# Optimization experiments

Hardware: AMD Instinct MI355X
Metric: run time of the kernel (lower is better)

The kernel has to match this reference:

```python
import jax, jax.numpy as jnp
import numpy as np
import math

EPS = 1e-5
BN_SCALE = 1.0 / math.sqrt(1.0 + EPS)  # eval BatchNorm with running mean 0, var 1


def _ln(x, g, b):
    m = jnp.mean(x, axis=-1, keepdims=True)
    v = jnp.mean((x - m) ** 2, axis=-1, keepdims=True)
    return (x - m) * jax.lax.rsqrt(v + EPS) * g + b


def _swish(x):
    return x * jax.nn.sigmoid(x)


def _ffn(x, ng, nb, w1, b1, w2, b2):
    h = _ln(x, ng, nb)
    h = _swish(h @ w1.T + b1)
    return h @ w2.T + b2


def _mhsa(x, a_ng, a_nb, qkv_w, qkv_b, rel_w, out_w, out_b):
    B, T, D = x.shape
    H, hd = rel_w.shape  # rel_pos_proj: Linear(head_dim, num_heads), weight [H, hd]
    h = _ln(x, a_ng, a_nb)
    qkv = (h @ qkv_w.T + qkv_b).reshape(B, T, 3, H, hd)
    q = qkv[:, :, 0].transpose(0, 2, 1, 3)  # [B,H,T,hd]
    k = qkv[:, :, 1].transpose(0, 2, 1, 3)
    v = qkv[:, :, 2].transpose(0, 2, 1, 3)
    scores = jnp.einsum('bhqd,bhkd->bhqk', q, k) * (hd ** -0.5)
    # relative sinusoidal PE over 2T-1 offsets
    pos = jnp.arange(-(T - 1), T, dtype=x.dtype)[:, None]
    div = jnp.exp(jnp.arange(0, hd, 2, dtype=x.dtype) * (-math.log(10000.0) / hd))
    ang = pos * div  # [2T-1, hd/2]
    pe = jnp.zeros((2 * T - 1, hd), dtype=x.dtype)
    pe = pe.at[:, 0::2].set(jnp.sin(ang)).at[:, 1::2].set(jnp.cos(ang))
    rel_bias = pe @ rel_w.T  # [2T-1, H]
    idx = jnp.arange(T)[:, None] - jnp.arange(T)[None, :] + (T - 1)  # [T,T]
    bias = rel_bias[idx].transpose(2, 0, 1)  # [H,T,T]
    attn = jax.nn.softmax(scores + bias[None], axis=-1)
    o = jnp.einsum('bhqk,bhkd->bhqd', attn, v).transpose(0, 2, 1, 3).reshape(B, T, D)
    return o @ out_w.T + out_b


def _conv(x, c_ng, c_nb, pw1_w, pw1_b, dw_w, dw_b, bn_g, bn_b, pw2_w, pw2_b):
    B, T, D = x.shape
    K = dw_w.shape[1]
    h = _ln(x, c_ng, c_nb)
    h = h @ pw1_w.T + pw1_b  # pointwise conv == linear, [B,T,2D]
    a, g = jnp.split(h, 2, axis=-1)
    h = a * jax.nn.sigmoid(g)  # GLU, [B,T,D]
    h = h.transpose(0, 2, 1)  # [B,D,T]
    h = jax.lax.conv_general_dilated(
        h, dw_w[:, None, :], window_strides=(1,), padding=[(K // 2, K // 2)],
        dimension_numbers=('NCH', 'OIH', 'NCH'), feature_group_count=D) + dw_b[:, None]
    h = h * (BN_SCALE * bn_g)[:, None] + bn_b[:, None]  # eval-mode BatchNorm1d
    h = _swish(h)
    h = h.transpose(0, 2, 1)  # [B,T,D]
    return h @ pw2_w.T + pw2_b


def _forward(x, g_ffn1, b_ffn1, g_mhsa, b_mhsa, g_conv, b_conv, g_ffn2, b_ffn2, g_out, b_out,
             f1_ng, f1_nb, f1_w1, f1_b1, f1_w2, f1_b2,
             f2_ng, f2_nb, f2_w1, f2_b1, f2_w2, f2_b2,
             a_ng, a_nb, qkv_w, qkv_b, rel_w, out_w, out_b,
             c_ng, c_nb, pw1_w, pw1_b, dw_w, dw_b, bn_g, bn_b, pw2_w, pw2_b):
    x = x + 0.5 * _ffn(_ln(x, g_ffn1, b_ffn1), f1_ng, f1_nb, f1_w1, f1_b1, f1_w2, f1_b2)
    x = x + _mhsa(_ln(x, g_mhsa, b_mhsa), a_ng, a_nb, qkv_w, qkv_b, rel_w, out_w, out_b)
    x = x + _conv(_ln(x, g_conv, b_conv), c_ng, c_nb, pw1_w, pw1_b, dw_w, dw_b, bn_g, bn_b, pw2_w, pw2_b)
    x = _ln(x + 0.5 * _ffn(_ln(x, g_ffn2, b_ffn2), f2_ng, f2_nb, f2_w1, f2_b1, f2_w2, f2_b2), g_out, b_out)
    return x


def setup_inputs() -> dict:
    key = jax.random.key(0)
    B, T, D, H, F, K = 8, 2048, 256, 4, 1024, 31
    ks = iter(jax.random.split(key, 16))
    w = lambda shape, s: jax.random.normal(next(ks), shape, jnp.float32) * s
    d = {}
    d['x'] = w((B, T, D), 1.0)
    for n in ['g_ffn1', 'g_mhsa', 'g_conv', 'g_ffn2', 'g_out', 'f1_ng', 'f2_ng', 'a_ng', 'c_ng', 'bn_g']:
        d[n] = jnp.ones((D,), jnp.float32)
    for n in ['b_ffn1', 'b_mhsa', 'b_conv', 'b_ffn2', 'b_out', 'f1_nb', 'f2_nb', 'a_nb', 'c_nb', 'bn_b']:
        d[n] = jnp.zeros((D,), jnp.float32)
    d['f1_w1'] = w((F, D), 0.05); d['f1_b1'] = jnp.zeros((F,), jnp.float32)
    d['f1_w2'] = w((D, F), 0.03); d['f1_b2'] = jnp.zeros((D,), jnp.float32)
    d['f2_w1'] = w((F, D), 0.05); d['f2_b1'] = jnp.zeros((F,), jnp.float32)
    d['f2_w2'] = w((D, F), 0.03); d['f2_b2'] = jnp.zeros((D,), jnp.float32)
    d['qkv_w'] = w((3 * D, D), 0.05); d['qkv_b'] = jnp.zeros((3 * D,), jnp.float32)
    d['rel_w'] = w((H, D // H), 0.05)
    d['out_w'] = w((D, D), 0.05); d['out_b'] = jnp.zeros((D,), jnp.float32)
    d['pw1_w'] = w((2 * D, D), 0.05); d['pw1_b'] = jnp.zeros((2 * D,), jnp.float32)
    d['dw_w'] = w((D, K), 0.1); d['dw_b'] = jnp.zeros((D,), jnp.float32)
    d['pw2_w'] = w((D, D), 0.05); d['pw2_b'] = jnp.zeros((D,), jnp.float32)
    return d


def reference(x, g_ffn1, b_ffn1, g_mhsa, b_mhsa, g_conv, b_conv, g_ffn2, b_ffn2, g_out, b_out,
              f1_ng, f1_nb, f1_w1, f1_b1, f1_w2, f1_b2,
              f2_ng, f2_nb, f2_w1, f2_b1, f2_w2, f2_b2,
              a_ng, a_nb, qkv_w, qkv_b, rel_w, out_w, out_b,
              c_ng, c_nb, pw1_w, pw1_b, dw_w, dw_b, bn_g, bn_b, pw2_w, pw2_b):
    return _forward(x, g_ffn1, b_ffn1, g_mhsa, b_mhsa, g_conv, b_conv, g_ffn2, b_ffn2, g_out, b_out,
                    f1_ng, f1_nb, f1_w1, f1_b1, f1_w2, f1_b2,
                    f2_ng, f2_nb, f2_w1, f2_b1, f2_w2, f2_b2,
                    a_ng, a_nb, qkv_w, qkv_b, rel_w, out_w, out_b,
                    c_ng, c_nb, pw1_w, pw1_b, dw_w, dw_b, bn_g, bn_b, pw2_w, pw2_b)
```

## Files before the change

kernel.cpp:

```cpp
#include <hip/hip_runtime.h>
#include <math.h>


typedef _Float16 half8 __attribute__((ext_vector_type(8)));
typedef _Float16 half4v __attribute__((ext_vector_type(4)));
typedef float floatx4 __attribute__((ext_vector_type(4)));

#define LN_EPS 1e-5f
#define BN_SCALE 0.9999950000374996f

__device__ __forceinline__ void async_copy16(const _Float16* g, _Float16* l) {
    __builtin_amdgcn_global_load_lds(
        (const __attribute__((address_space(1))) void*)g,
        (__attribute__((address_space(3))) void*)l, 16, 0, 0);
}

__global__ __launch_bounds__(256) void cast_kernel(const float* __restrict__ s,
                                                   _Float16* __restrict__ d, int n) {
    int i = blockIdx.x * 256 + threadIdx.x;
    if (i < n) d[i] = (_Float16)s[i];
}

__global__ __launch_bounds__(256) void cast_pw1_kernel(const float* __restrict__ w,
        const float* __restrict__ b, _Float16* __restrict__ wp, float* __restrict__ bp) {
    int i = blockIdx.x * 256 + threadIdx.x;
    int p = i >> 8, c = i & 255;
    int chunk = p >> 4, within = p & 15;
    int orig = ((chunk & 1) ? 256 : 0) + (chunk >> 1) * 16 + within;
    wp[i] = (_Float16)w[orig * 256 + c];
    if (c == 0) bp[p] = b[orig];
}

__global__ __launch_bounds__(256) void ln2_kernel(const float* __restrict__ x,
        const float* __restrict__ g1, const float* __restrict__ b1,
        const float* __restrict__ g2, const float* __restrict__ b2,
        _Float16* __restrict__ y) {
    int wave = threadIdx.x >> 6, lane = threadIdx.x & 63;
    size_t row = (size_t)blockIdx.x * 4 + wave;
    float4 v = ((const float4*)(x + row * 256))[lane];
    float s = v.x + v.y + v.z + v.w;
    float s2 = v.x * v.x + v.y * v.y + v.z * v.z + v.w * v.w;
    #pragma unroll
    for (int m = 1; m < 64; m <<= 1) { s += __shfl_xor(s, m, 64); s2 += __shfl_xor(s2, m, 64); }
    float mean = s * (1.f / 256.f);
    float var = s2 * (1.f / 256.f) - mean * mean;
    float rs = rsqrtf(var + LN_EPS);
    int c0 = lane * 4;
    float y0 = (v.x - mean) * rs * g1[c0 + 0] + b1[c0 + 0];
    float y1 = (v.y - mean) * rs * g1[c0 + 1] + b1[c0 + 1];
    float y2 = (v.z - mean) * rs * g1[c0 + 2] + b1[c0 + 2];
    float y3 = (v.w - mean) * rs * g1[c0 + 3] + b1[c0 + 3];
    float t = y0 + y1 + y2 + y3;
    float t2 = y0 * y0 + y1 * y1 + y2 * y2 + y3 * y3;
    #pragma unroll
    for (int m = 1; m < 64; m <<= 1) { t += __shfl_xor(t, m, 64); t2 += __shfl_xor(t2, m, 64); }
    float mean2 = t * (1.f / 256.f);
    float var2 = t2 * (1.f / 256.f) - mean2 * mean2;
    float rs2 = rsqrtf(var2 + LN_EPS);
    half4v o;
    o[0] = (_Float16)((y0 - mean2) * rs2 * g2[c0 + 0] + b2[c0 + 0]);
    o[1] = (_Float16)((y1 - mean2) * rs2 * g2[c0 + 1] + b2[c0 + 1]);
    o[2] = (_Float16)((y2 - mean2) * rs2 * g2[c0 + 2] + b2[c0 + 2]);
    o[3] = (_Float16)((y3 - mean2) * rs2 * g2[c0 + 3] + b2[c0 + 3]);
    *(half4v*)(y + row * 256 + c0) = o;
}

__global__ __launch_bounds__(256) void ln1_kernel(const float* __restrict__ x,
        const float* __restrict__ g, const float* __restrict__ b,
        float* __restrict__ y) {
    int wave = threadIdx.x >> 6, lane = threadIdx.x & 63;
    size_t row = (size_t)blockIdx.x * 4 + wave;
    float4 v = ((const float4*)(x + row * 256))[lane];
    float s = v.x + v.y + v.z + v.w;
    float s2 = v.x * v.x + v.y * v.y + v.z * v.z + v.w * v.w;
    #pragma unroll
    for (int m = 1; m < 64; m <<= 1) { s += __shfl_xor(s, m, 64); s2 += __shfl_xor(s2, m, 64); }
    float mean = s * (1.f / 256.f);
    float var = s2 * (1.f / 256.f) - mean * mean;
    float rs = rsqrtf(var + LN_EPS);
    int c0 = lane * 4;
    float4 o;
    o.x = (v.x - mean) * rs * g[c0 + 0] + b[c0 + 0];
    o.y = (v.y - mean) * rs * g[c0 + 1] + b[c0 + 1];
    o.z = (v.z - mean) * rs * g[c0 + 2] + b[c0 + 2];
    o.w = (v.w - mean) * rs * g[c0 + 3] + b[c0 + 3];
    ((float4*)(y + row * 256))[lane] = o;
}

template <int EPI>
__global__ __launch_bounds__(256) void gemm128(
        const _Float16* __restrict__ A, const _Float16* __restrict__ W,
        const float* __restrict__ bias, const float* __restrict__ res, float alpha,
        float* __restrict__ outf, _Float16* __restrict__ outh,
        _Float16* __restrict__ outv, int N, int K) {
    __shared__ _Float16 As[128 * 64];
    __shared__ _Float16 Ws[128 * 64];
    int tid = threadIdx.x, wave = tid >> 6, lane = tid & 63;
    int n0 = blockIdx.x * 128, m0 = blockIdx.y * 128;
    int wr = wave >> 1, wc = wave & 1;
    floatx4 acc[4][4] = {};
    int l15 = lane & 15, kq = (lane >> 4) * 8, quad = lane >> 4;
    int srow = wave * 32 + (lane >> 3);
    int scol = (lane & 7) * 8;
    const _Float16* Aptr = A + (size_t)(m0 + srow) * K + scol;
    const _Float16* Wptr = W + (size_t)(n0 + srow) * K + scol;
    _Float16* AsBase = As + wave * 32 * 64;
    _Float16* WsBase = Ws + wave * 32 * 64;
    for (int k0 = 0; k0 < K; k0 += 64) {
        __syncthreads();
        #pragma unroll
        for (int i = 0; i < 4; i++)
            async_copy16(Aptr + k0 + (size_t)i * 8 * K, AsBase + i * 8 * 64);
        #pragma unroll
        for (int i = 0; i < 4; i++)
            async_copy16(Wptr + k0 + (size_t)i * 8 * K, WsBase + i * 8 * 64);
        __syncthreads();
        #pragma unroll
        for (int ks = 0; ks < 2; ks++) {
            half8 a[4], b[4];
            #pragma unroll
            for (int i = 0; i < 4; i++)
                a[i] = *(const half8*)&As[(wr * 64 + i * 16 + l15) * 64 + ks * 32 + kq];
            #pragma unroll
            for (int j = 0; j < 4; j++)
                b[j] = *(const half8*)&Ws[(wc * 64 + j * 16 + l15) * 64 + ks * 32 + kq];
            #pragma unroll
            for (int i = 0; i < 4; i++)
                #pragma unroll
                for (int j = 0; j < 4; j++)
                    acc[i][j] = __builtin_amdgcn_mfma_f32_16x16x32_f16(a[i], b[j], acc[i][j], 0, 0, 0);
        }
    }
    #pragma unroll
    for (int i = 0; i < 4; i++) {
        int mrow = m0 + wr * 64 + i * 16 + quad * 4;
        if (EPI == 2) {
            #pragma unroll
            for (int jp = 0; jp < 2; jp++) {
                int j = 2 * jp;
                int Pa = n0 + wc * 64 + j * 16 + l15;
                float ba = bias[Pa], bg = bias[Pa + 16];
                int d = ((Pa >> 5) << 4) + l15;
                #pragma unroll
                for (int r = 0; r < 4; r++) {
                    float av = acc[i][j][r] + ba;
                    float gv = acc[i][j + 1][r] + bg;
                    outh[(size_t)(mrow + r) * 256 + d] = (_Float16)(av / (1.f + __expf(-gv)));
                }
            }
        } else if (EPI == 5) {
            #pragma unroll
            for (int j = 0; j < 4; j++) {
                int n = n0 + wc * 64 + j * 16 + l15;
                float bv = bias[n];
                if (n0 < 512) {
                    #pragma unroll
                    for (int r = 0; r < 4; r++)
                        outh[(size_t)(mrow + r) * N + n] = (_Float16)(acc[i][j][r] + bv);
                } else {
                    int hv = (n - 512) >> 6, d = (n - 512) & 63;
                    int bb = m0 >> 11;
                    int t0 = (m0 & 2047) + wr * 64 + i * 16 + quad * 4;
                    half4v vv;
                    #pragma unroll
                    for (int r = 0; r < 4; r++) vv[r] = (_Float16)(acc[i][j][r] + bv);
                    *(half4v*)(outv + ((size_t)((bb * 4 + hv) * 64 + d)) * 2048 + t0) = vv;
                }
            }
        } else {
            #pragma unroll
            for (int j = 0; j < 4; j++) {
                int n = n0 + wc * 64 + j * 16 + l15;
                float bv = bias[n];
                #pragma unroll
                for (int r = 0; r < 4; r++) {
                    float c = acc[i][j][r] + bv;
                    size_t m = (size_t)(mrow + r);
                    if (EPI == 1) {
                        outh[m * N + n] = (_Float16)(c / (1.f + __expf(-c)));
                    } else {
                        outf[m * N + n] = res[m * N + n] + alpha * c;
                    }
                }
            }
        }
    }
}

__global__ __launch_bounds__(256) void relbias_kernel(const float* __restrict__ rel_w,
                                                      float* __restrict__ rb) {
    int i = blockIdx.x * 256 + threadIdx.x;
    if (i >= 4095 * 4) return;
    int p = i >> 2, h = i & 3;
    float pos = (float)(p - 2047);
    const float c = -logf(10000.f) / 64.f;
    float acc = 0.f;
    for (int k = 0; k < 32; k++) {
        float dv = expf((float)(2 * k) * c);
        float ang = pos * dv;
        acc += sinf(ang) * rel_w[h * 64 + 2 * k] + cosf(ang) * rel_w[h * 64 + 2 * k + 1];
    }
    rb[h * 4095 + p] = acc;
}

__global__ __launch_bounds__(256) void attn_kernel(const _Float16* __restrict__ qkv,
        const _Float16* __restrict__ vtg, const float* __restrict__ rb,
        _Float16* __restrict__ o) {
    const int T = 2048;
    int qt = blockIdx.x, h = blockIdx.y, b = blockIdx.z;
    int tid = threadIdx.x, wave = tid >> 6, lane = tid & 63;
    __shared__ __align__(16) _Float16 Qs[64][72];
    __shared__ __align__(16) _Float16 Ks[64][72];
    __shared__ __align__(16) _Float16 Vt[64][72];
    __shared__ __align__(16) _Float16 Ps[4][16][72];
    __shared__ float bias_lds[128];

    size_t qrow0 = (size_t)b * T + qt * 64;
    #pragma unroll
    for (int i = 0; i < 2; i++) {
        int idx = tid + 256 * i, r = idx >> 3, sg = idx & 7;
        *(float4*)(&Qs[r][sg * 8]) = *(const float4*)(qkv + (qrow0 + r) * 768 + h * 64 + sg * 8);
    }
    __syncthreads();
    int kq = (lane >> 4) * 8;
    int l15 = lane & 15;
    int quad = lane >> 4;
    half8 qa[2];
    qa[0] = *(const half8*)(&Qs[wave * 16 + l15][kq]);
    qa[1] = *(const half8*)(&Qs[wave * 16 + l15][32 + kq]);
    half8 ones;
    #pragma unroll
    for (int j = 0; j < 8; j++) ones[j] = (_Float16)1.f;

    floatx4 oacc[4] = {};
    floatx4 lacc = {};
    const float* rbh = rb + h * 4095;
    const _Float16* vbase = vtg + ((size_t)(b * 4 + h)) * 64 * 2048;

    for (int kt = 0; kt < 32; kt++) {
        __syncthreads();
        #pragma unroll
        for (int i = 0; i < 2; i++) {
            int idx = tid + 256 * i, r = idx >> 3, sg = idx & 7;
            *(float4*)(&Ks[r][sg * 8]) =
                *(const float4*)(qkv + ((size_t)b * T + kt * 64 + r) * 768 + 256 + h * 64 + sg * 8);
            *(float4*)(&Vt[r][sg * 8]) =
                *(const float4*)(vbase + (size_t)r * 2048 + kt * 64 + sg * 8);
        }
        if (tid < 128) {
            int base = qt * 64 - kt * 64 + 1984;
            bias_lds[tid] = rbh[min(base + tid, 4094)];
        }
        __syncthreads();
        floatx4 s[4] = {};
        #pragma unroll
        for (int ks = 0; ks < 2; ks++)
            #pragma unroll
            for (int nt = 0; nt < 4; nt++) {
                half8 bb = *(const half8*)(&Ks[nt * 16 + l15][ks * 32 + kq]);
                s[nt] = __builtin_amdgcn_mfma_f32_16x16x32_f16(qa[ks], bb, s[nt], 0, 0, 0);
            }
        int rloc = quad * 4;
        #pragma unroll
        for (int nt = 0; nt < 4; nt++) {
            int krel = nt * 16 + l15;
            #pragma unroll
            for (int r = 0; r < 4; r++) {
                float sv = s[nt][r] * 0.125f + bias_lds[wave * 16 + rloc + r - krel + 63];
                float p = __expf(fminf(sv, 11.f));
                Ps[wave][rloc + r][nt * 16 + l15] = (_Float16)p;
            }
        }
        #pragma unroll
        for (int ks = 0; ks < 2; ks++) {
            half8 pa = *(const half8*)(&Ps[wave][l15][ks * 32 + kq]);
            lacc = __builtin_amdgcn_mfma_f32_16x16x32_f16(pa, ones, lacc, 0, 0, 0);
            #pragma unroll
            for (int nt = 0; nt < 4; nt++) {
                half8 bb = *(const half8*)(&Vt[nt * 16 + l15][ks * 32 + kq]);
                oacc[nt] = __builtin_amdgcn_mfma_f32_16x16x32_f16(pa, bb, oacc[nt], 0, 0, 0);
            }
        }
    }
    size_t orow0 = qrow0 + wave * 16 + quad * 4;
    #pragma unroll
    for (int r = 0; r < 4; r++) {
        float inv = 1.f / lacc[r];
        #pragma unroll
        for (int nt = 0; nt < 4; nt++)
            o[(orow0 + r) * 256 + h * 64 + nt * 16 + l15] = (_Float16)(oacc[nt][r] * inv);
    }
}

__global__ __launch_bounds__(256) void dwconv_kernel(const _Float16* __restrict__ glu,
        const float* __restrict__ dw_w, const float* __restrict__ dw_b,
        const float* __restrict__ bn_g, const float* __restrict__ bn_b,
        _Float16* __restrict__ out) {
    const int T = 2048;
    int d = threadIdx.x;
    int b = blockIdx.y, t0 = blockIdx.x * 128;
    const _Float16* base = glu + ((size_t)b * T) * 256 + d;
    float w[31], win[31];
    #pragma unroll
    for (int j = 0; j < 31; j++) w[j] = dw_w[d * 31 + j];
    #pragma unroll
    for (int j = 0; j < 31; j++) {
        int tt = t0 - 15 + j;
        win[j] = (tt >= 0 && tt < T) ? (float)base[(size_t)tt * 256] : 0.f;
    }
    float dwb = dw_b[d];
    float bns = BN_SCALE * bn_g[d];
    float bnb = bn_b[d];
    size_t orow = ((size_t)b * T) * 256 + d;
    for (int i = 0; i < 128; i++) {
        int t = t0 + i;
        float acc = dwb;
        #pragma unroll
        for (int j = 0; j < 31; j++) acc += win[j] * w[j];
        float bn = acc * bns + bnb;
        out[orow + (size_t)t * 256] = (_Float16)(bn / (1.f + __expf(-bn)));
        #pragma unroll
        for (int j = 0; j < 30; j++) win[j] = win[j + 1];
        int tn = t + 16;
        win[30] = (tn < T) ? (float)base[(size_t)tn * 256] : 0.f;
    }
}

extern "C" void kernel_launch(void* const* d_in, const int* in_sizes, int n_in,
                              void* d_out, int out_size, void* d_ws, size_t ws_size,
                              hipStream_t stream) {
    (void)in_sizes; (void)n_in; (void)out_size; (void)ws_size;
    const float* x      = (const float*)d_in[0];
    const float* g_ffn1 = (const float*)d_in[1];
    const float* g_mhsa = (const float*)d_in[2];
    const float* g_conv = (const float*)d_in[3];
    const float* g_ffn2 = (const float*)d_in[4];
    const float* g_out  = (const float*)d_in[5];
    const float* f1_ng  = (const float*)d_in[6];
    const float* f2_ng  = (const float*)d_in[7];
    const float* a_ng   = (const float*)d_in[8];
    const float* c_ng   = (const float*)d_in[9];
    const float* bn_g   = (const float*)d_in[10];
    const float* b_ffn1 = (const float*)d_in[11];
    const float* b_mhsa = (const float*)d_in[12];
    const float* b_conv = (const float*)d_in[13];
    const float* b_ffn2 = (const float*)d_in[14];
    const float* b_out  = (const float*)d_in[15];
    const float* f1_nb  = (const float*)d_in[16];
    const float* f2_nb  = (const float*)d_in[17];
    const float* a_nb   = (const float*)d_in[18];
    const float* c_nb   = (const float*)d_in[19];
    const float* bn_b   = (const float*)d_in[20];
    const float* f1_w1  = (const float*)d_in[21];
    const float* f1_b1  = (const float*)d_in[22];
    const float* f1_w2  = (const float*)d_in[23];
    const float* f1_b2  = (const float*)d_in[24];
    const float* f2_w1  = (const float*)d_in[25];
    const float* f2_b1  = (const float*)d_in[26];
    const float* f2_w2  = (const float*)d_in[27];
    const float* f2_b2  = (const float*)d_in[28];
    const float* qkv_w  = (const float*)d_in[29];
    const float* qkv_b  = (const float*)d_in[30];
    const float* rel_w  = (const float*)d_in[31];
    const float* out_w  = (const float*)d_in[32];
    const float* out_b  = (const float*)d_in[33];
    const float* pw1_w  = (const float*)d_in[34];
    const float* pw1_b  = (const float*)d_in[35];
    const float* dw_w   = (const float*)d_in[36];
    const float* dw_b   = (const float*)d_in[37];
    const float* pw2_w  = (const float*)d_in[38];
    const float* pw2_b  = (const float*)d_in[39];

    const int BT = 16384;
    char* ws = (char*)d_ws;
    size_t off = 0;
    auto alloc = [&](size_t bytes) -> char* {
        char* p = ws + off;
        off += (bytes + 255) & ~(size_t)255;
        return p;
    };
    _Float16* wf1w1 = (_Float16*)alloc(262144 * 2);
    _Float16* wf1w2 = (_Float16*)alloc(262144 * 2);
    _Float16* wf2w1 = (_Float16*)alloc(262144 * 2);
    _Float16* wf2w2 = (_Float16*)alloc(262144 * 2);
    _Float16* wqkv  = (_Float16*)alloc(196608 * 2);
    _Float16* wout  = (_Float16*)alloc(65536 * 2);
    _Float16* wpw1  = (_Float16*)alloc(131072 * 2);
    float* pb1      = (float*)alloc(512 * 4);
    _Float16* wpw2  = (_Float16*)alloc(65536 * 2);
    float* rbbuf    = (float*)alloc(4 * 4095 * 4);
    float* xA       = (float*)alloc((size_t)BT * 256 * 4);
    float* xB       = (float*)alloc((size_t)BT * 256 * 4);
    _Float16* t16   = (_Float16*)alloc((size_t)BT * 256 * 2);
    char* R1        = alloc((size_t)BT * 1024 * 2);
    _Float16* vtg   = (_Float16*)alloc((size_t)8 * 4 * 64 * 2048 * 2);
    _Float16* glu16 = (_Float16*)alloc((size_t)BT * 256 * 2);
    _Float16* o16   = (_Float16*)alloc((size_t)BT * 256 * 2);
    _Float16* h16   = (_Float16*)R1;
    _Float16* qkv16 = (_Float16*)R1;

    cast_kernel<<<1024, 256, 0, stream>>>(f1_w1, wf1w1, 262144);
    cast_kernel<<<1024, 256, 0, stream>>>(f1_w2, wf1w2, 262144);
    cast_kernel<<<1024, 256, 0, stream>>>(f2_w1, wf2w1, 262144);
    cast_kernel<<<1024, 256, 0, stream>>>(f2_w2, wf2w2, 262144);
    cast_kernel<<<768, 256, 0, stream>>>(qkv_w, wqkv, 196608);
    cast_kernel<<<256, 256, 0, stream>>>(out_w, wout, 65536);
    cast_pw1_kernel<<<512, 256, 0, stream>>>(pw1_w, pw1_b, wpw1, pb1);
    cast_kernel<<<256, 256, 0, stream>>>(pw2_w, wpw2, 65536);
    relbias_kernel<<<64, 256, 0, stream>>>(rel_w, rbbuf);

    ln2_kernel<<<BT / 4, 256, 0, stream>>>(x, g_ffn1, b_ffn1, f1_ng, f1_nb, t16);
    gemm128<1><<<dim3(8, 128), 256, 0, stream>>>(t16, wf1w1, f1_b1, nullptr, 0.f, nullptr, h16, nullptr, 1024, 256);
    gemm128<3><<<dim3(2, 128), 256, 0, stream>>>(h16, wf1w2, f1_b2, x, 0.5f, xA, nullptr, nullptr, 256, 1024);
    ln2_kernel<<<BT / 4, 256, 0, stream>>>(xA, g_mhsa, b_mhsa, a_ng, a_nb, t16);
    gemm128<5><<<dim3(6, 128), 256, 0, stream>>>(t16, wqkv, qkv_b, nullptr, 0.f, nullptr, qkv16, vtg, 768, 256);
    attn_kernel<<<dim3(32, 4, 8), 256, 0, stream>>>(qkv16, vtg, rbbuf, o16);
    gemm128<3><<<dim3(2, 128), 256, 0, stream>>>(o16, wout, out_b, xA, 1.f, xB, nullptr, nullptr, 256, 256);
    ln2_kernel<<<BT / 4, 256, 0, stream>>>(xB, g_conv, b_conv, c_ng, c_nb, t16);
    gemm128<2><<<dim3(4, 128), 256, 0, stream>>>(t16, wpw1, pb1, nullptr, 0.f, nullptr, glu16, nullptr, 512, 256);
    dwconv_kernel<<<dim3(16, 8), 256, 0, stream>>>(glu16, dw_w, dw_b, bn_g, bn_b, t16);
    gemm128<3><<<dim3(2, 128), 256, 0, stream>>>(t16, wpw2, pw2_b, xB, 1.f, xA, nullptr, nullptr, 256, 256);
    ln2_kernel<<<BT / 4, 256, 0, stream>>>(xA, g_ffn2, b_ffn2, f2_ng, f2_nb, t16);
    gemm128<1><<<dim3(8, 128), 256, 0, stream>>>(t16, wf2w1, f2_b1, nullptr, 0.f, nullptr, h16, nullptr, 1024, 256);
    gemm128<3><<<dim3(2, 128), 256, 0, stream>>>(h16, wf2w2, f2_b2, xA, 0.5f, xB, nullptr, nullptr, 256, 1024);
    ln1_kernel<<<BT / 4, 256, 0, stream>>>(xB, g_out, b_out, (float*)d_out);
}
```

Measured before the change: 510.3 us.

## Double attention query tile per block, batch weight casts into one launch

The attention kernel now processes 128 query rows per block (two 16-row sub-tiles per wave), so each K/V tile loaded into LDS is reused twice and the grid halves. K and V fragments are hoisted into registers once per tile. The softmax switches to exp2 by folding log2(e) into the score scale and the precomputed relative bias. Seven separate weight-cast launches are merged into one kernel that picks its segment from the index. The cost is higher register pressure and only 512 attention blocks, which may lower occupancy.

```diff
diff --git a/kernel.cpp b/kernel.cpp
--- a/kernel.cpp
+++ b/kernel.cpp
@@ -8,6 +8,7 @@
 
 #define LN_EPS 1e-5f
 #define BN_SCALE 0.9999950000374996f
+#define LOG2E 1.44269504f
 
 __device__ __forceinline__ void async_copy16(const _Float16* g, _Float16* l) {
     __builtin_amdgcn_global_load_lds(
@@ -15,10 +16,15 @@
         (__attribute__((address_space(3))) void*)l, 16, 0, 0);
 }
 
-__global__ __launch_bounds__(256) void cast_kernel(const float* __restrict__ s,
-                                                   _Float16* __restrict__ d, int n) {
+struct CastJobs { const float* s[7]; _Float16* d[7]; };
+__global__ __launch_bounds__(256) void cast_all(CastJobs j) {
     int i = blockIdx.x * 256 + threadIdx.x;
-    if (i < n) d[i] = (_Float16)s[i];
+    int seg, base;
+    if (i < 1048576)      { seg = i >> 18; base = seg << 18; }
+    else if (i < 1245184) { seg = 4; base = 1048576; }
+    else if (i < 1310720) { seg = 5; base = 1245184; }
+    else                  { seg = 6; base = 1310720; }
+    j.d[seg][i - base] = (_Float16)j.s[seg][i - base];
 }
 
 __global__ __launch_bounds__(256) void cast_pw1_kernel(const float* __restrict__ w,
@@ -200,7 +206,7 @@
         float ang = pos * dv;
         acc += sinf(ang) * rel_w[h * 64 + 2 * k] + cosf(ang) * rel_w[h * 64 + 2 * k + 1];
     }
-    rb[h * 4095 + p] = acc;
+    rb[h * 4095 + p] = acc * LOG2E;
 }
 
 __global__ __launch_bounds__(256) void attn_kernel(const _Float16* __restrict__ qkv,
@@ -209,86 +215,109 @@
     const int T = 2048;
     int qt = blockIdx.x, h = blockIdx.y, b = blockIdx.z;
     int tid = threadIdx.x, wave = tid >> 6, lane = tid & 63;
-    __shared__ __align__(16) _Float16 Qs[64][72];
+    __shared__ __align__(16) _Float16 Qs[128][72];
     __shared__ __align__(16) _Float16 Ks[64][72];
     __shared__ __align__(16) _Float16 Vt[64][72];
-    __shared__ __align__(16) _Float16 Ps[4][16][72];
-    __shared__ float bias_lds[128];
-
-    size_t qrow0 = (size_t)b * T + qt * 64;
-    #pragma unroll
-    for (int i = 0; i < 2; i++) {
+    __shared__ __align__(16) _Float16 Ps[4][32][72];
+    __shared__ float bias_lds[192];
+
+    int l15 = lane & 15, quad = lane >> 4, kq = quad * 8;
+    size_t qrow0 = (size_t)b * T + qt * 128;
+    #pragma unroll
+    for (int i = 0; i < 4; i++) {
         int idx = tid + 256 * i, r = idx >> 3, sg = idx & 7;
         *(float4*)(&Qs[r][sg * 8]) = *(const float4*)(qkv + (qrow0 + r) * 768 + h * 64 + sg * 8);
     }
     __syncthreads();
-    int kq = (lane >> 4) * 8;
-    int l15 = lane & 15;
-    int quad = lane >> 4;
-    half8 qa[2];
-    qa[0] = *(const half8*)(&Qs[wave * 16 + l15][kq]);
-    qa[1] = *(const half8*)(&Qs[wave * 16 + l15][32 + kq]);
+    half8 qa[2][2];
+    #pragma unroll
+    for (int u = 0; u < 2; u++)
+        #pragma unroll
+        for (int ks = 0; ks < 2; ks++)
+            qa[u][ks] = *(const half8*)(&Qs[u * 64 + wave * 16 + l15][ks * 32 + kq]);
     half8 ones;
     #pragma unroll
     for (int j = 0; j < 8; j++) ones[j] = (_Float16)1.f;
 
-    floatx4 oacc[4] = {};
-    floatx4 lacc = {};
+    floatx4 oacc[2][4] = {};
+    floatx4 lacc[2] = {};
     const float* rbh = rb + h * 4095;
     const _Float16* vbase = vtg + ((size_t)(b * 4 + h)) * 64 * 2048;
+    const _Float16* kbase = qkv + ((size_t)b * T) * 768 + 256 + h * 64;
 
     for (int kt = 0; kt < 32; kt++) {
         __syncthreads();
         #pragma unroll
         for (int i = 0; i < 2; i++) {
             int idx = tid + 256 * i, r = idx >> 3, sg = idx & 7;
-            *(float4*)(&Ks[r][sg * 8]) =
-                *(const float4*)(qkv + ((size_t)b * T + kt * 64 + r) * 768 + 256 + h * 64 + sg * 8);
-            *(float4*)(&Vt[r][sg * 8]) =
-                *(const float4*)(vbase + (size_t)r * 2048 + kt * 64 + sg * 8);
+            *(float4*)(&Ks[r][sg * 8]) = *(const float4*)(kbase + (size_t)(kt * 64 + r) * 768 + sg * 8);
+            *(float4*)(&Vt[r][sg * 8]) = *(const float4*)(vbase + (size_t)r * 2048 + kt * 64 + sg * 8);
         }
-        if (tid < 128) {
-            int base = qt * 64 - kt * 64 + 1984;
+        if (tid < 192) {
+            int base = qt * 128 - kt * 64 + 1984;
             bias_lds[tid] = rbh[min(base + tid, 4094)];
         }
         __syncthreads();
-        floatx4 s[4] = {};
+        half8 kf[2][4];
         #pragma unroll
         for (int ks = 0; ks < 2; ks++)
             #pragma unroll
+            for (int nt = 0; nt < 4; nt++)
+                kf[ks][nt] = *(const half8*)(&Ks[nt * 16 + l15][ks * 32 + kq]);
+        floatx4 s[2][4];
+        #pragma unroll
+        for (int u = 0; u < 2; u++)
+            #pragma unroll
             for (int nt = 0; nt < 4; nt++) {
-                half8 bb = *(const half8*)(&Ks[nt * 16 + l15][ks * 32 + kq]);
-                s[nt] = __builtin_amdgcn_mfma_f32_16x16x32_f16(qa[ks], bb, s[nt], 0, 0, 0);
-            }
-        int rloc = quad * 4;
-        #pragma unroll
-        for (int nt = 0; nt < 4; nt++) {
-            int krel = nt * 16 + l15;
-            #pragma unroll
-            for (int r = 0; r < 4; r++) {
-                float sv = s[nt][r] * 0.125f + bias_lds[wave * 16 + rloc + r - krel + 63];
-                float p = __expf(fminf(sv, 11.f));
-                Ps[wave][rloc + r][nt * 16 + l15] = (_Float16)p;
-            }
+                floatx4 z = {};
+                s[u][nt] = z;
+            }
+        #pragma unroll
+        for (int u = 0; u < 2; u++)
+            #pragma unroll
+            for (int ks = 0; ks < 2; ks++)
+                #pragma unroll
+                for (int nt = 0; nt < 4; nt++)
+                    s[u][nt] = __builtin_amdgcn_mfma_f32_16x16x32_f16(qa[u][ks], kf[ks][nt], s[u][nt], 0, 0, 0);
+        #pragma unroll
+        for (int u = 0; u < 2; u++)
+            #pragma unroll
+            for (int nt = 0; nt < 4; nt++) {
+                int cb = u * 64 + wave * 16 + quad * 4 - (nt * 16 + l15) + 63;
+                #pragma unroll
+                for (int r = 0; r < 4; r++) {
+                    float sv = s[u][nt][r] * (0.125f * LOG2E) + bias_lds[cb + r];
+                    Ps[wave][u * 16 + quad * 4 + r][nt * 16 + l15] =
+                        (_Float16)exp2f(fminf(sv, 15.86f));
+                }
+            }
+        half8 vf[2][4];
+        #pragma unroll
+        for (int ks = 0; ks < 2; ks++)
+            #pragma unroll
+            for (int nt = 0; nt < 4; nt++)
+                vf[ks][nt] = *(const half8*)(&Vt[nt * 16 + l15][ks * 32 + kq]);
+        #pragma unroll
+        for (int u = 0; u < 2; u++)
+            #pragma unroll
+            for (int ks = 0; ks < 2; ks++) {
+                half8 pa = *(const half8*)(&Ps[wave][u * 16 + l15][ks * 32 + kq]);
+                lacc[u] = __builtin_amdgcn_mfma_f32_16x16x32_f16(pa, ones, lacc[u], 0, 0, 0);
+                #pragma unroll
+                for (int nt = 0; nt < 4; nt++)
+                    oacc[u][nt] = __builtin_amdgcn_mfma_f32_16x16x32_f16(pa, vf[ks][nt], oacc[u][nt], 0, 0, 0);
+            }
+    }
+    #pragma unroll
+    for (int u = 0; u < 2; u++) {
+        size_t orow0 = qrow0 + u * 64 + wave * 16 + quad * 4;
+        #pragma unroll
+        for (int r = 0; r < 4; r++) {
+            float inv = 1.f / lacc[u][r];
+            #pragma unroll
+            for (int nt = 0; nt < 4; nt++)
+                o[(orow0 + r) * 256 + h * 64 + nt * 16 + l15] = (_Float16)(oacc[u][nt][r] * inv);
         }
-        #pragma unroll
-        for (int ks = 0; ks < 2; ks++) {
-            half8 pa = *(const half8*)(&Ps[wave][l15][ks * 32 + kq]);
-            lacc = __builtin_amdgcn_mfma_f32_16x16x32_f16(pa, ones, lacc, 0, 0, 0);
-            #pragma unroll
-            for (int nt = 0; nt < 4; nt++) {
-                half8 bb = *(const half8*)(&Vt[nt * 16 + l15][ks * 32 + kq]);
-                oacc[nt] = __builtin_amdgcn_mfma_f32_16x16x32_f16(pa, bb, oacc[nt], 0, 0, 0);
-            }
-        }
-    }
-    size_t orow0 = qrow0 + wave * 16 + quad * 4;
-    #pragma unroll
-    for (int r = 0; r < 4; r++) {
-        float inv = 1.f / lacc[r];
-        #pragma unroll
-        for (int nt = 0; nt < 4; nt++)
-            o[(orow0 + r) * 256 + h * 64 + nt * 16 + l15] = (_Float16)(oacc[nt][r] * inv);
     }
 }
 
@@ -399,14 +428,16 @@
     _Float16* h16   = (_Float16*)R1;
     _Float16* qkv16 = (_Float16*)R1;
 
-    cast_kernel<<<1024, 256, 0, stream>>>(f1_w1, wf1w1, 262144);
-    cast_kernel<<<1024, 256, 0, stream>>>(f1_w2, wf1w2, 262144);
-    cast_kernel<<<1024, 256, 0, stream>>>(f2_w1, wf2w1, 262144);
-    cast_kernel<<<1024, 256, 0, stream>>>(f2_w2, wf2w2, 262144);
-    cast_kernel<<<768, 256, 0, stream>>>(qkv_w, wqkv, 196608);
-    cast_kernel<<<256, 256, 0, stream>>>(out_w, wout, 65536);
+    CastJobs cj;
+    cj.s[0] = f1_w1; cj.d[0] = wf1w1;
+    cj.s[1] = f1_w2; cj.d[1] = wf1w2;
+    cj.s[2] = f2_w1; cj.d[2] = wf2w1;
+    cj.s[3] = f2_w2; cj.d[3] = wf2w2;
+    cj.s[4] = qkv_w; cj.d[4] = wqkv;
+    cj.s[5] = out_w; cj.d[5] = wout;
+    cj.s[6] = pw2_w; cj.d[6] = wpw2;
+    cast_all<<<5376, 256, 0, stream>>>(cj);
     cast_pw1_kernel<<<512, 256, 0, stream>>>(pw1_w, pw1_b, wpw1, pb1);
-    cast_kernel<<<256, 256, 0, stream>>>(pw2_w, wpw2, 65536);
     relbias_kernel<<<64, 256, 0, stream>>>(rel_w, rbbuf);
 
     ln2_kernel<<<BT / 4, 256, 0, stream>>>(x, g_ffn1, b_ffn1, f1_ng, f1_nb, t16);
@@ -414,7 +445,7 @@
     gemm128<3><<<dim3(2, 128), 256, 0, stream>>>(h16, wf1w2, f1_b2, x, 0.5f, xA, nullptr, nullptr, 256, 1024);
     ln2_kernel<<<BT / 4, 256, 0, stream>>>(xA, g_mhsa, b_mhsa, a_ng, a_nb, t16);
     gemm128<5><<<dim3(6, 128), 256, 0, stream>>>(t16, wqkv, qkv_b, nullptr, 0.f, nullptr, qkv16, vtg, 768, 256);
-    attn_kernel<<<dim3(32, 4, 8), 256, 0, stream>>>(qkv16, vtg, rbbuf, o16);
+    attn_kernel<<<dim3(16, 4, 8), 256, 0, stream>>>(qkv16, vtg, rbbuf, o16);
     gemm128<3><<<dim3(2, 128), 256, 0, stream>>>(o16, wout, out_b, xA, 1.f, xB, nullptr, nullptr, 256, 256);
     ln2_kernel<<<BT / 4, 256, 0, stream>>>(xB, g_conv, b_conv, c_ng, c_nb, t16);
     gemm128<2><<<dim3(4, 128), 256, 0, stream>>>(t16, wpw1, pb1, nullptr, 0.f, nullptr, glu16, nullptr, 512, 256);
```

Result: no change. 507.0 us (-0.7%).
